# Kernel optimization log

Hardware: AMD Instinct MI355X
Metric: run time of the kernel (lower is better)

The kernel has to match this reference:

```python
import jax, jax.numpy as jnp
import numpy as np

VOC, EMB, C, H, W, ANS = 10000, 300, 24, 8, 8, 1000
HID = 500          # lstm_hidden_size
GH = 100           # g_mlp hidden
B, L = 64, 32
O = H * W          # obj_num
CONCAT = 2 * C + HID  # 548


def setup_inputs() -> dict:
    key = jax.random.key(0)
    ks = jax.random.split(key, 20)
    inp = {}
    inp["sent_batch"] = jax.random.randint(ks[0], (B, L), 0, VOC)
    inp["conv_map_batch"] = jax.random.normal(ks[1], (B, C, H, W), jnp.float32)
    inp["sents_lengths"] = jax.random.randint(ks[2], (B,), 1, L + 1)
    # embedding table with padding_idx=0 zeroed
    emb = jax.random.normal(ks[3], (VOC, EMB), jnp.float32) * 0.02
    inp["embed_table"] = emb.at[0].set(0.0)
    # forward-direction LSTM params (torch gate order i,f,g,o)
    s_ih = 1.0 / np.sqrt(HID)
    inp["W_ih"] = jax.random.uniform(ks[4], (4 * HID, EMB), jnp.float32, -s_ih, s_ih)
    inp["W_hh"] = jax.random.uniform(ks[5], (4 * HID, HID), jnp.float32, -s_ih, s_ih)
    inp["b_ih"] = jax.random.uniform(ks[6], (4 * HID,), jnp.float32, -s_ih, s_ih)
    inp["b_hh"] = jax.random.uniform(ks[7], (4 * HID,), jnp.float32, -s_ih, s_ih)
    # random (non-learned) LSTM initial state, as torch.rand in init_hidden
    inp["h0"] = jax.random.uniform(ks[8], (B, HID), jnp.float32)
    inp["c0"] = jax.random.uniform(ks[9], (B, HID), jnp.float32)
    def lin(k, o, i):
        s = 1.0 / np.sqrt(i)
        kw, kb = jax.random.split(k)
        return (jax.random.uniform(kw, (o, i), jnp.float32, -s, s),
                jax.random.uniform(kb, (o,), jnp.float32, -s, s))
    inp["g1_w"], inp["g1_b"] = lin(ks[10], GH, CONCAT)
    inp["g2_w"], inp["g2_b"] = lin(ks[11], GH, GH)
    inp["f1_w"], inp["f1_b"] = lin(ks[12], GH, GH)
    inp["f2_w"], inp["f2_b"] = lin(ks[13], ANS, GH)
    return inp


def _lstm_final_h(emb, lengths, W_ih, W_hh, b_ih, b_hh, h0, c0):
    # emb: (B, L, EMB); returns final forward hidden at t = length-1 per example
    xs = jnp.swapaxes(emb, 0, 1)  # (L, B, EMB)
    ts = jnp.arange(emb.shape[1])
    bias = b_ih + b_hh
    def step(carry, inp):
        h, c = carry
        xt, t = inp
        gates = xt @ W_ih.T + h @ W_hh.T + bias
        i, f, g, o = jnp.split(gates, 4, axis=-1)
        i, f, o = jax.nn.sigmoid(i), jax.nn.sigmoid(f), jax.nn.sigmoid(o)
        g = jnp.tanh(g)
        c_new = f * c + i * g
        h_new = o * jnp.tanh(c_new)
        m = (t < lengths)[:, None]
        return (jnp.where(m, h_new, h), jnp.where(m, c_new, c)), None
    (h_T, _), _ = jax.lax.scan(step, (h0, c0), (xs, ts))
    return h_T  # (B, HID)


def reference(sent_batch, conv_map_batch, sents_lengths, embed_table,
              W_ih, W_hh, b_ih, b_hh, h0, c0,
              g1_w, g1_b, g2_w, g2_b, f1_w, f1_b, f2_w, f2_b):
    emb = embed_table[sent_batch]  # (B, L, EMB)
    q = _lstm_final_h(emb, sents_lengths, W_ih, W_hh, b_ih, b_hh, h0, c0)  # (B, HID)
    obj = jnp.transpose(conv_map_batch, (0, 2, 3, 1)).reshape(B, O, C)  # (B, O, C)
    # g_mlp layer 1, split to avoid materializing (B, O^2, 548):
    # pair (i,j): cat(q, obj_j, obj_i) -> partial sums broadcast-added
    q_part = q @ g1_w[:, :HID].T                    # (B, GH)
    j_part = obj @ g1_w[:, HID:HID + C].T           # (B, O, GH) -- conv_expand_1 block
    i_part = obj @ g1_w[:, HID + C:].T              # (B, O, GH) -- conv_expand_2 block
    h1 = jax.nn.relu(q_part[:, None, None, :] + i_part[:, :, None, :]
                     + j_part[:, None, :, :] + g1_b)  # (B, O, O, GH)
    h2 = jax.nn.relu(h1 @ g2_w.T + g2_b)              # (B, O, O, GH)
    g_sum = h2.sum(axis=(1, 2))                       # (B, GH)
    f = jax.nn.relu(g_sum @ f1_w.T + f1_b)
    f = jax.nn.relu(f @ f2_w.T + f2_b)                # (B, ANS)
    return jax.nn.log_softmax(f, axis=-1)
```

## Files before the change

### kernel.cpp

```cpp
#include <hip/hip_runtime.h>
#include <cmath>

#define BATCH 64
#define SEQL  32
#define EMBD  300
#define HIDD  500
#define NOBJ  64
#define GHID  100
#define ANSN  1000
#define MCOL  2048

#define GRP    4
#define GBATCH 16
#define BPG    25
#define UPB8   20
#define NBLK   (GRP*BPG)
#define SLOTP  32

#define KPADX  328
#define TCH    4

typedef _Float16 half8 __attribute__((ext_vector_type(8)));
typedef float    f32x4 __attribute__((ext_vector_type(4)));

__device__ __forceinline__ float sigmf(float x){ return 1.f/(1.f+expf(-x)); }

__device__ __forceinline__ unsigned long long ld_cc8(const unsigned long long* p){
    return __hip_atomic_load(p, __ATOMIC_RELAXED, __HIP_MEMORY_SCOPE_AGENT);
}
__device__ __forceinline__ void st_cc8(_Float16* p, unsigned long long v){
    __hip_atomic_store((unsigned long long*)p, v, __ATOMIC_RELAXED, __HIP_MEMORY_SCOPE_AGENT);
}

__global__ __launch_bounds__(256, 1) void k_xg2(
    const int* __restrict__ sent, const float* __restrict__ table,
    const float* __restrict__ Wih, const float* __restrict__ b_ih,
    const float* __restrict__ b_hh, float* __restrict__ xgT, int* __restrict__ slots)
{
    __shared__ _Float16 Sh[64*KPADX];
    __shared__ int sidx[TCH][64];
    int tid = threadIdx.x;
    int tc = blockIdx.x;
    int n0 = blockIdx.y * 64;
    int w = tid >> 6, lane = tid & 63;
    int rA = lane & 15, kb = lane >> 4;

    if (tc == 0 && blockIdx.y == 0 && tid < NBLK)
        __hip_atomic_store(slots + tid*SLOTP, 0, __ATOMIC_RELAXED, __HIP_MEMORY_SCOPE_AGENT);

    for (int i = tid; i < TCH*64; i += 256){
        int tt = i >> 6, b = i & 63;
        sidx[tt][b] = sent[b*SEQL + tc*TCH + tt];
    }
    for (int i = tid; i < 64*75; i += 256){
        int n = i / 75, c4 = i - (i/75)*75;
        float4 v = {0.f,0.f,0.f,0.f};
        if (n0 + n < 2000)
            v = *(const float4*)(Wih + (size_t)(n0+n)*300 + c4*4);
        _Float16* dst = &Sh[n*KPADX + c4*4];
        dst[0]=(_Float16)v.x; dst[1]=(_Float16)v.y; dst[2]=(_Float16)v.z; dst[3]=(_Float16)v.w;
    }
    for (int i = tid; i < 64*20; i += 256){
        int n = i / 20, k = 300 + (i - (i/20)*20);
        Sh[n*KPADX + k] = (_Float16)0.f;
    }
    __syncthreads();
    half8 areg[10];
    #pragma unroll
    for (int ks = 0; ks < 10; ++ks)
        areg[ks] = *(const half8*)&Sh[(w*16 + rA)*KPADX + ks*32 + kb*8];
    float biasr[4];
    #pragma unroll
    for (int r = 0; r < 4; ++r){
        int n = n0 + w*16 + kb*4 + r;
        biasr[r] = (n < 2000) ? b_ih[n] + b_hh[n] : 0.f;
    }
    __syncthreads();

    for (int tt = 0; tt < TCH; ++tt){
        for (int i = tid; i < 64*75; i += 256){
            int m = i / 75, c4 = i - (i/75)*75;
            float4 v = *(const float4*)(table + (size_t)sidx[tt][m]*300 + c4*4);
            _Float16* dst = &Sh[m*KPADX + c4*4];
            dst[0]=(_Float16)v.x; dst[1]=(_Float16)v.y; dst[2]=(_Float16)v.z; dst[3]=(_Float16)v.w;
        }
        for (int i = tid; i < 64*20; i += 256){
            int m = i / 20, k = 300 + (i - (i/20)*20);
            Sh[m*KPADX + k] = (_Float16)0.f;
        }
        __syncthreads();

        f32x4 acc[4] = {};
        #pragma unroll
        for (int ks = 0; ks < 10; ++ks){
            #pragma unroll
            for (int mc = 0; mc < 4; ++mc){
                half8 bf = *(const half8*)&Sh[(mc*16 + rA)*KPADX + ks*32 + kb*8];
                acc[mc] = __builtin_amdgcn_mfma_f32_16x16x32_f16(areg[ks], bf, acc[mc], 0, 0, 0);
            }
        }
        #pragma unroll
        for (int r = 0; r < 4; ++r){
            int n = n0 + w*16 + kb*4 + r;
            if (n < 2000){
                #pragma unroll
                for (int mc = 0; mc < 4; ++mc)
                    xgT[(size_t)n*MCOL + (tc*TCH+tt)*64 + mc*16 + rA] = acc[mc][r] + biasr[r];
            }
        }
        __syncthreads();
    }
}

__device__ __forceinline__ void gbarA(int* slots, int grp, int ub, int seq)
{
    __syncthreads();
    if (threadIdx.x == 0)
        __hip_atomic_store(slots + (grp*BPG + ub)*SLOTP, seq,
                           __ATOMIC_RELAXED, __HIP_MEMORY_SCOPE_AGENT);
    if (threadIdx.x < BPG){
        int* s = slots + (grp*BPG + threadIdx.x)*SLOTP;
        while (__hip_atomic_load(s, __ATOMIC_RELAXED, __HIP_MEMORY_SCOPE_AGENT) < seq)
            __builtin_amdgcn_s_sleep(1);
    }
    asm volatile("" ::: "memory");
    __syncthreads();
}

__global__ __launch_bounds__(320, 1) void k_lstm_v9(
    _Float16* __restrict__ hF, float* __restrict__ hqB,
    const float* __restrict__ xgT, const float* __restrict__ Whh,
    const float* __restrict__ h0, const float* __restrict__ c0,
    const int* __restrict__ lens, int* __restrict__ slots)
{
    __shared__ _Float16 Wl[80*512];
    __shared__ float    gl[4*80*16];
    __shared__ _Float16 hout[16*UPB8];

    int tid = threadIdx.x, bid = blockIdx.x;
    int grp = bid / BPG, ub = bid - grp*BPG;
    int u0  = ub * UPB8;
    int w   = tid >> 6, lane = tid & 63;

    int pb  = tid & 15, puu = tid >> 4;
    int pu  = u0 + puu;
    int gb  = grp*GBATCH + pb;
    float cprev = c0[gb*HIDD + pu];
    float hprev = h0[gb*HIDD + pu];
    int   mylen = lens[gb];
    hout[pb*UPB8 + puu] = (_Float16)hprev;

    for (int i = tid; i < 80*512; i += 320){
        int m = i >> 9, k = i & 511;
        int g = m / UPB8, uu = m - g*UPB8;
        float v = (k < HIDD) ? Whh[(size_t)(g*HIDD + u0 + uu)*HIDD + k] : 0.f;
        int off = (i*2) ^ ((m & 7) << 4);
        *(_Float16*)((char*)Wl + off) = (_Float16)v;
    }
    __syncthreads();
    if (tid < 80){
        int b = tid / 5, q = tid - (tid/5)*5;
        unsigned long long v = *(const unsigned long long*)((const char*)hout + b*40 + q*8);
        st_cc8(hF + ((size_t)(1*GRP + grp)*GBATCH + b)*512 + u0 + q*4, v);
    }
    if (ub == 0 && tid >= 128 && tid < 224){
        int j = tid - 128;
        int buf = j / 48, r = j - buf*48;
        int b = r / 3, q = r - (r/3)*3;
        st_cc8(hF + ((size_t)(buf*GRP + grp)*GBATCH + b)*512 + 500 + q*4, 0ULL);
    }
    gbarA(slots, grp, ub, 1);

    const int mA = lane & 15, kb = lane >> 4;

    for (int t = 0; t < SEQL; ++t){
        const _Float16* hsrc = hF + (size_t)(((t&1)^1)*GRP + grp)*GBATCH*512;

        float xgv[4];
        #pragma unroll
        for (int g = 0; g < 4; ++g)
            xgv[g] = xgT[(size_t)(g*HIDD + pu)*MCOL + t*64 + gb];

        if (w < 4){
            half8 bf[4];
            #pragma unroll
            for (int ks4 = 0; ks4 < 4; ++ks4){
                int ke = (w*4 + ks4)*32 + kb*8;
                const unsigned long long* p =
                    (const unsigned long long*)(hsrc + mA*512 + ke);
                union { unsigned long long q[2]; half8 h; } u;
                u.q[0] = ld_cc8(p);
                u.q[1] = ld_cc8(p + 1);
                bf[ks4] = u.h;
            }
            f32x4 acc[5] = {};
            #pragma unroll
            for (int rt = 0; rt < 5; ++rt){
                #pragma unroll
                for (int ks4 = 0; ks4 < 4; ++ks4){
                    int kByte = (w*4 + ks4)*64 + kb*16;
                    int m = rt*16 + mA;
                    int aOff = (m*1024 + kByte) ^ ((m & 7) << 4);
                    half8 af = *(const half8*)((const char*)Wl + aOff);
                    acc[rt] = __builtin_amdgcn_mfma_f32_16x16x32_f16(af, bf[ks4], acc[rt], 0, 0, 0);
                }
            }
            #pragma unroll
            for (int rt = 0; rt < 5; ++rt)
                #pragma unroll
                for (int r = 0; r < 4; ++r)
                    gl[(w*80 + rt*16 + kb*4 + r)*16 + mA] = acc[rt][r];
        }
        __syncthreads();

        {
            float g4[4];
            #pragma unroll
            for (int g = 0; g < 4; ++g){
                int row = g*UPB8 + puu;
                float s = gl[(0*80 + row)*16 + pb] + gl[(1*80 + row)*16 + pb]
                        + gl[(2*80 + row)*16 + pb] + gl[(3*80 + row)*16 + pb];
                s += xgv[g];
                g4[g] = s;
            }
            float si = sigmf(g4[0]), sf = sigmf(g4[1]);
            float tg = tanhf(g4[2]), so = sigmf(g4[3]);
            float cn = sf*cprev + si*tg;
            float hn = so*tanhf(cn);
            if (t < mylen){ cprev = cn; hprev = hn; }
            hout[pb*UPB8 + puu] = (_Float16)hprev;
            if (t == SEQL-1) hqB[(size_t)gb*512 + pu] = hprev;
        }
        if (t < SEQL-1){
            __syncthreads();
            if (tid < 80){
                int b = tid / 5, q = tid - (tid/5)*5;
                unsigned long long v = *(const unsigned long long*)((const char*)hout + b*40 + q*8);
                st_cc8(hF + ((size_t)((t&1)*GRP + grp)*GBATCH + b)*512 + u0 + q*4, v);
            }
            gbarA(slots, grp, ub, t + 2);
        }
    }
}

__global__ __launch_bounds__(256, 1) void k_pair2(
    const float* __restrict__ hqB, const float* __restrict__ conv,
    const float* __restrict__ g1w, const float* __restrict__ g1b,
    const float* __restrict__ g2w, const float* __restrict__ g2b,
    float* __restrict__ part)
{
    __shared__ float    convl[24][64];
    __shared__ float    g1ij[100][48];
    __shared__ float    hb[512];
    __shared__ float    qpl[112];
    __shared__ float    jpl[NOBJ][132];
    __shared__ float    basel[16][132];
    __shared__ _Float16 g2h[112][136];
    __shared__ float    redx[4][112];

    int b  = blockIdx.x >> 2;
    int ic = blockIdx.x & 3;
    int tid = threadIdx.x;
    int w = tid >> 6, lane = tid & 63;
    int ncol = lane & 15, kb = lane >> 4;

    for (int i = tid; i < 24*64; i += 256)
        convl[i>>6][i&63] = conv[((size_t)b*24 + (i>>6))*64 + (i&63)];
    for (int i = tid; i < 100*48; i += 256){
        int n = i/48, c = i - (i/48)*48;
        g1ij[n][c] = g1w[(size_t)n*548 + 500 + c];
    }
    for (int i = tid; i < 512; i += 256) hb[i] = hqB[(size_t)b*512 + i];
    for (int i = tid; i < 112*136; i += 256){
        int n = i/136, k = i - (i/136)*136;
        g2h[n][k] = (n < 100 && k < 100) ? (_Float16)g2w[n*GHID + k] : (_Float16)0.f;
    }
    __syncthreads();

    if (tid < 100){
        const float4* wr = (const float4*)(g1w + (size_t)tid*548);
        float s = g1b[tid];
        #pragma unroll 5
        for (int k4 = 0; k4 < 125; ++k4){
            float4 v = wr[k4];
            s += v.x*hb[k4*4] + v.y*hb[k4*4+1] + v.z*hb[k4*4+2] + v.w*hb[k4*4+3];
        }
        qpl[tid] = s;
    }
    for (int i = tid; i < NOBJ*100; i += 256){
        int o = i / 100, n = i - (i/100)*100;
        float sj = 0.f;
        #pragma unroll
        for (int c = 0; c < 24; ++c) sj += convl[c][o] * g1ij[n][c];
        jpl[o][n] = sj;
    }
    for (int i = tid; i < NOBJ*32; i += 256) jpl[i>>5][100 + (i&31)] = 0.f;
    __syncthreads();

    for (int i = tid; i < 16*132; i += 256){
        int il = i / 132, k = i - (i/132)*132;
        float v = 0.f;
        if (k < 100){
            float si = 0.f;
            int o = ic*16 + il;
            #pragma unroll
            for (int c = 0; c < 24; ++c) si += convl[c][o] * g1ij[k][24+c];
            v = qpl[k] + si;
        }
        basel[il][k] = v;
    }
    float gb7[7];
    #pragma unroll
    for (int nt = 0; nt < 7; ++nt){
        int n = nt*16 + ncol;
        gb7[nt] = (n < 100) ? g2b[n] : 0.f;
    }
    __syncthreads();

    f32x4 sacc[7] = {};
    #pragma unroll
    for (int it = 0; it < 4; ++it){
        int il = w*4 + it;
        #pragma unroll
        for (int jc = 0; jc < 4; ++jc){
            f32x4 acc[7] = {};
            int jrow = jc*16 + ncol;
            #pragma unroll
            for (int ks = 0; ks < 4; ++ks){
                int k0 = ks*32 + kb*8;
                const float* jpp = &jpl[jrow][k0];
                const float* bpp = &basel[il][k0];
                half8 af;
                #pragma unroll
                for (int e = 0; e < 8; ++e)
                    af[e] = (_Float16)fmaxf(jpp[e] + bpp[e], 0.f);
                #pragma unroll
                for (int nt = 0; nt < 7; ++nt){
                    half8 bf = *(const half8*)&g2h[nt*16 + ncol][k0];
                    acc[nt] = __builtin_amdgcn_mfma_f32_16x16x32_f16(af, bf, acc[nt], 0, 0, 0);
                }
            }
            #pragma unroll
            for (int nt = 0; nt < 7; ++nt)
                #pragma unroll
                for (int r = 0; r < 4; ++r)
                    sacc[nt][r] += fmaxf(acc[nt][r] + gb7[nt], 0.f);
        }
    }
    #pragma unroll
    for (int nt = 0; nt < 7; ++nt){
        float s = sacc[nt][0] + sacc[nt][1] + sacc[nt][2] + sacc[nt][3];
        s += __shfl_xor(s, 16);
        s += __shfl_xor(s, 32);
        if (lane < 16) redx[w][nt*16 + lane] = s;
    }
    __syncthreads();
    if (tid < 100){
        float p = redx[0][tid] + redx[1][tid] + redx[2][tid] + redx[3][tid];
        part[(size_t)(b*4 + ic)*GHID + tid] = p;
    }
}

__global__ __launch_bounds__(256) void k_final(const float* __restrict__ part, const float* __restrict__ f1w,
               const float* __restrict__ f1b, const float* __restrict__ f2w,
               const float* __restrict__ f2b, float* __restrict__ out)
{
    int b = blockIdx.x;
    int tid = threadIdx.x;
    __shared__ float gs[GHID];
    __shared__ float fh[GHID];
    __shared__ float lg[ANSN];
    __shared__ float red[4], red2[4];
    if (tid < GHID){
        float s = 0.f;
        for (int ic = 0; ic < 4; ++ic) s += part[((size_t)b*4 + ic)*GHID + tid];
        gs[tid] = s;
    }
    __syncthreads();
    if (tid < GHID){
        float s = f1b[tid];
        const float* w = f1w + tid*GHID;
        for (int k = 0; k < GHID; ++k) s += gs[k]*w[k];
        fh[tid] = fmaxf(s, 0.f);
    }
    __syncthreads();
    for (int n = tid; n < ANSN; n += 256){
        float s = f2b[n];
        const float* w = f2w + (size_t)n*GHID;
        for (int k = 0; k < GHID; ++k) s += fh[k]*w[k];
        lg[n] = fmaxf(s, 0.f);
    }
    __syncthreads();
    float mx = -1e30f;
    for (int n = tid; n < ANSN; n += 256) mx = fmaxf(mx, lg[n]);
    #pragma unroll
    for (int off = 32; off > 0; off >>= 1) mx = fmaxf(mx, __shfl_xor(mx, off));
    if ((tid & 63) == 0) red[tid >> 6] = mx;
    __syncthreads();
    mx = fmaxf(fmaxf(red[0], red[1]), fmaxf(red[2], red[3]));
    float se = 0.f;
    for (int n = tid; n < ANSN; n += 256) se += expf(lg[n]-mx);
    #pragma unroll
    for (int off = 32; off > 0; off >>= 1) se += __shfl_xor(se, off);
    if ((tid & 63) == 0) red2[tid >> 6] = se;
    __syncthreads();
    se = red2[0]+red2[1]+red2[2]+red2[3];
    float lse = logf(se);
    for (int n = tid; n < ANSN; n += 256) out[(size_t)b*ANSN + n] = lg[n] - mx - lse;
}

extern "C" void kernel_launch(void* const* d_in, const int* in_sizes, int n_in,
                              void* d_out, int out_size, void* d_ws, size_t ws_size,
                              hipStream_t stream)
{
    const int*   sent  = (const int*)  d_in[0];
    const float* conv  = (const float*)d_in[1];
    const int*   lens  = (const int*)  d_in[2];
    const float* table = (const float*)d_in[3];
    const float* W_ih  = (const float*)d_in[4];
    const float* W_hh  = (const float*)d_in[5];
    const float* b_ih  = (const float*)d_in[6];
    const float* b_hh  = (const float*)d_in[7];
    const float* h0    = (const float*)d_in[8];
    const float* c0    = (const float*)d_in[9];
    const float* g1_w  = (const float*)d_in[10];
    const float* g1_b  = (const float*)d_in[11];
    const float* g2_w  = (const float*)d_in[12];
    const float* g2_b  = (const float*)d_in[13];
    const float* f1_w  = (const float*)d_in[14];
    const float* f1_b  = (const float*)d_in[15];
    const float* f2_w  = (const float*)d_in[16];
    const float* f2_b  = (const float*)d_in[17];
    float* out = (float*)d_out;

    float* ws   = (float*)d_ws;
    int*   slots= (int*)d_ws;
    _Float16* hF = (_Float16*)(ws + 16384);
    float* hqB  = ws + 16384 + 32768;
    float* xgT  = hqB + 64*512;
    float* part = xgT + (size_t)4*HIDD*MCOL;

    {
        dim3 g(SEQL/TCH, 32);
        k_xg2<<<g, 256, 0, stream>>>(sent, table, W_ih, b_ih, b_hh, xgT, slots);
    }

    k_lstm_v9<<<NBLK, 320, 0, stream>>>(hF, hqB, xgT, W_hh, h0, c0, lens, slots);

    k_pair2<<<BATCH*4, 256, 0, stream>>>(hqB, conv, g1_w, g1_b, g2_w, g2_b, part);

    k_final<<<BATCH, 256, 0, stream>>>(part, f1_w, f1_b, f2_w, f2_b, out);
}
```

Before: 258.3 us.

## Fuse input-gate GEMM into LSTM kernel with per-chunk readiness flags

Merges the x·W_ih precompute kernel into the persistent LSTM kernel. Extra blocks beyond the 100 recurrence blocks compute the input gates for 4-timestep chunks and bump a per-chunk counter. Recurrence blocks wait on that counter before each chunk, so the input projection overlaps the serial recurrence instead of running before it. The risk is deadlock if the recurrence blocks are not co-resident or are scheduled ahead of the producer blocks. It also adds a memset launch plus atomic loads and stores on xgT.

```diff
diff --git a/kernel.cpp b/kernel.cpp
--- a/kernel.cpp
+++ b/kernel.cpp
@@ -15,6 +15,7 @@
 #define BPG    25
 #define UPB8   20
 #define NBLK   (GRP*BPG)
+#define NXG    256
 #define SLOTP  32
 
 #define KPADX  328
@@ -31,85 +32,11 @@
 __device__ __forceinline__ void st_cc8(_Float16* p, unsigned long long v){
     __hip_atomic_store((unsigned long long*)p, v, __ATOMIC_RELAXED, __HIP_MEMORY_SCOPE_AGENT);
 }
-
-__global__ __launch_bounds__(256, 1) void k_xg2(
-    const int* __restrict__ sent, const float* __restrict__ table,
-    const float* __restrict__ Wih, const float* __restrict__ b_ih,
-    const float* __restrict__ b_hh, float* __restrict__ xgT, int* __restrict__ slots)
-{
-    __shared__ _Float16 Sh[64*KPADX];
-    __shared__ int sidx[TCH][64];
-    int tid = threadIdx.x;
-    int tc = blockIdx.x;
-    int n0 = blockIdx.y * 64;
-    int w = tid >> 6, lane = tid & 63;
-    int rA = lane & 15, kb = lane >> 4;
-
-    if (tc == 0 && blockIdx.y == 0 && tid < NBLK)
-        __hip_atomic_store(slots + tid*SLOTP, 0, __ATOMIC_RELAXED, __HIP_MEMORY_SCOPE_AGENT);
-
-    for (int i = tid; i < TCH*64; i += 256){
-        int tt = i >> 6, b = i & 63;
-        sidx[tt][b] = sent[b*SEQL + tc*TCH + tt];
-    }
-    for (int i = tid; i < 64*75; i += 256){
-        int n = i / 75, c4 = i - (i/75)*75;
-        float4 v = {0.f,0.f,0.f,0.f};
-        if (n0 + n < 2000)
-            v = *(const float4*)(Wih + (size_t)(n0+n)*300 + c4*4);
-        _Float16* dst = &Sh[n*KPADX + c4*4];
-        dst[0]=(_Float16)v.x; dst[1]=(_Float16)v.y; dst[2]=(_Float16)v.z; dst[3]=(_Float16)v.w;
-    }
-    for (int i = tid; i < 64*20; i += 256){
-        int n = i / 20, k = 300 + (i - (i/20)*20);
-        Sh[n*KPADX + k] = (_Float16)0.f;
-    }
-    __syncthreads();
-    half8 areg[10];
-    #pragma unroll
-    for (int ks = 0; ks < 10; ++ks)
-        areg[ks] = *(const half8*)&Sh[(w*16 + rA)*KPADX + ks*32 + kb*8];
-    float biasr[4];
-    #pragma unroll
-    for (int r = 0; r < 4; ++r){
-        int n = n0 + w*16 + kb*4 + r;
-        biasr[r] = (n < 2000) ? b_ih[n] + b_hh[n] : 0.f;
-    }
-    __syncthreads();
-
-    for (int tt = 0; tt < TCH; ++tt){
-        for (int i = tid; i < 64*75; i += 256){
-            int m = i / 75, c4 = i - (i/75)*75;
-            float4 v = *(const float4*)(table + (size_t)sidx[tt][m]*300 + c4*4);
-            _Float16* dst = &Sh[m*KPADX + c4*4];
-            dst[0]=(_Float16)v.x; dst[1]=(_Float16)v.y; dst[2]=(_Float16)v.z; dst[3]=(_Float16)v.w;
-        }
-        for (int i = tid; i < 64*20; i += 256){
-            int m = i / 20, k = 300 + (i - (i/20)*20);
-            Sh[m*KPADX + k] = (_Float16)0.f;
-        }
-        __syncthreads();
-
-        f32x4 acc[4] = {};
-        #pragma unroll
-        for (int ks = 0; ks < 10; ++ks){
-            #pragma unroll
-            for (int mc = 0; mc < 4; ++mc){
-                half8 bf = *(const half8*)&Sh[(mc*16 + rA)*KPADX + ks*32 + kb*8];
-                acc[mc] = __builtin_amdgcn_mfma_f32_16x16x32_f16(areg[ks], bf, acc[mc], 0, 0, 0);
-            }
-        }
-        #pragma unroll
-        for (int r = 0; r < 4; ++r){
-            int n = n0 + w*16 + kb*4 + r;
-            if (n < 2000){
-                #pragma unroll
-                for (int mc = 0; mc < 4; ++mc)
-                    xgT[(size_t)n*MCOL + (tc*TCH+tt)*64 + mc*16 + rA] = acc[mc][r] + biasr[r];
-            }
-        }
-        __syncthreads();
-    }
+__device__ __forceinline__ float ld_cc4(const float* p){
+    return __hip_atomic_load(p, __ATOMIC_RELAXED, __HIP_MEMORY_SCOPE_AGENT);
+}
+__device__ __forceinline__ void st_cc4(float* p, float v){
+    __hip_atomic_store(p, v, __ATOMIC_RELAXED, __HIP_MEMORY_SCOPE_AGENT);
 }
 
 __device__ __forceinline__ void gbarA(int* slots, int grp, int ub, int seq)
@@ -127,20 +54,105 @@
     __syncthreads();
 }
 
-__global__ __launch_bounds__(320, 1) void k_lstm_v9(
-    _Float16* __restrict__ hF, float* __restrict__ hqB,
-    const float* __restrict__ xgT, const float* __restrict__ Whh,
-    const float* __restrict__ h0, const float* __restrict__ c0,
-    const int* __restrict__ lens, int* __restrict__ slots)
+__global__ __launch_bounds__(320, 1) void k_mega(
+    const int* __restrict__ sent, const float* __restrict__ table,
+    const float* __restrict__ Wih, const float* __restrict__ b_ih, const float* __restrict__ b_hh,
+    _Float16* __restrict__ hF, float* __restrict__ hqB, float* __restrict__ xgT,
+    const float* __restrict__ Whh, const float* __restrict__ h0, const float* __restrict__ c0,
+    const int* __restrict__ lens, int* __restrict__ slots, int* __restrict__ xgdone)
 {
-    __shared__ _Float16 Wl[80*512];
-    __shared__ float    gl[4*80*16];
-    __shared__ _Float16 hout[16*UPB8];
+    __shared__ __align__(16) char smem[103040];
 
     int tid = threadIdx.x, bid = blockIdx.x;
+    int w = tid >> 6, lane = tid & 63;
+
+    if (bid >= NBLK){
+        _Float16* Sh  = (_Float16*)smem;
+        int*      sidx= (int*)(smem + 41984);
+        int xb = bid - NBLK;
+        int tc = xb >> 5;
+        int n0 = (xb & 31) * 64;
+        int rA = lane & 15, kb = lane >> 4;
+
+        for (int i = tid; i < TCH*64; i += 320){
+            int tt = i >> 6, b = i & 63;
+            sidx[tt*64 + b] = sent[b*SEQL + tc*TCH + tt];
+        }
+        for (int i = tid; i < 64*75; i += 320){
+            int n = i / 75, c4 = i - (i/75)*75;
+            float4 v = {0.f,0.f,0.f,0.f};
+            if (n0 + n < 2000)
+                v = *(const float4*)(Wih + (size_t)(n0+n)*300 + c4*4);
+            _Float16* dst = &Sh[n*KPADX + c4*4];
+            dst[0]=(_Float16)v.x; dst[1]=(_Float16)v.y; dst[2]=(_Float16)v.z; dst[3]=(_Float16)v.w;
+        }
+        for (int i = tid; i < 64*20; i += 320){
+            int n = i / 20, k = 300 + (i - (i/20)*20);
+            Sh[n*KPADX + k] = (_Float16)0.f;
+        }
+        __syncthreads();
+        half8 areg[10];
+        float biasr[4];
+        if (w < 4){
+            #pragma unroll
+            for (int ks = 0; ks < 10; ++ks)
+                areg[ks] = *(const half8*)&Sh[(w*16 + rA)*KPADX + ks*32 + kb*8];
+            #pragma unroll
+            for (int r = 0; r < 4; ++r){
+                int n = n0 + w*16 + kb*4 + r;
+                biasr[r] = (n < 2000) ? b_ih[n] + b_hh[n] : 0.f;
+            }
+        }
+        __syncthreads();
+
+        for (int tt = 0; tt < TCH; ++tt){
+            for (int i = tid; i < 64*75; i += 320){
+                int m = i / 75, c4 = i - (i/75)*75;
+                float4 v = *(const float4*)(table + (size_t)sidx[tt*64 + m]*300 + c4*4);
+                _Float16* dst = &Sh[m*KPADX + c4*4];
+                dst[0]=(_Float16)v.x; dst[1]=(_Float16)v.y; dst[2]=(_Float16)v.z; dst[3]=(_Float16)v.w;
+            }
+            for (int i = tid; i < 64*20; i += 320){
+                int m = i / 20, k = 300 + (i - (i/20)*20);
+                Sh[m*KPADX + k] = (_Float16)0.f;
+            }
+            __syncthreads();
+
+            if (w < 4){
+                f32x4 acc[4] = {};
+                #pragma unroll
+                for (int ks = 0; ks < 10; ++ks){
+                    #pragma unroll
+                    for (int mc = 0; mc < 4; ++mc){
+                        half8 bf = *(const half8*)&Sh[(mc*16 + rA)*KPADX + ks*32 + kb*8];
+                        acc[mc] = __builtin_amdgcn_mfma_f32_16x16x32_f16(areg[ks], bf, acc[mc], 0, 0, 0);
+                    }
+                }
+                #pragma unroll
+                for (int r = 0; r < 4; ++r){
+                    int n = n0 + w*16 + kb*4 + r;
+                    if (n < 2000){
+                        #pragma unroll
+                        for (int mc = 0; mc < 4; ++mc)
+                            st_cc4(xgT + (size_t)n*MCOL + (tc*TCH+tt)*64 + mc*16 + rA,
+                                   acc[mc][r] + biasr[r]);
+                    }
+                }
+            }
+            __syncthreads();
+        }
+        if (tid == 0)
+            __hip_atomic_fetch_add(xgdone + tc*SLOTP, 1,
+                                   __ATOMIC_RELAXED, __HIP_MEMORY_SCOPE_AGENT);
+        return;
+    }
+
+    _Float16* Wl  = (_Float16*)smem;
+    float*    gl  = (float*)(smem + 81920);
+    _Float16* hout= (_Float16*)(smem + 102400);
+
     int grp = bid / BPG, ub = bid - grp*BPG;
     int u0  = ub * UPB8;
-    int w   = tid >> 6, lane = tid & 63;
 
     int pb  = tid & 15, puu = tid >> 4;
     int pu  = u0 + puu;
@@ -174,12 +186,22 @@
     const int mA = lane & 15, kb = lane >> 4;
 
     for (int t = 0; t < SEQL; ++t){
+        if ((t & 3) == 0){
+            if (tid == 0){
+                const int* f = xgdone + (t >> 2)*SLOTP;
+                while (__hip_atomic_load(f, __ATOMIC_RELAXED, __HIP_MEMORY_SCOPE_AGENT) < 32)
+                    __builtin_amdgcn_s_sleep(1);
+            }
+            asm volatile("" ::: "memory");
+            __syncthreads();
+        }
+
         const _Float16* hsrc = hF + (size_t)(((t&1)^1)*GRP + grp)*GBATCH*512;
 
         float xgv[4];
         #pragma unroll
         for (int g = 0; g < 4; ++g)
-            xgv[g] = xgT[(size_t)(g*HIDD + pu)*MCOL + t*64 + gb];
+            xgv[g] = ld_cc4(xgT + (size_t)(g*HIDD + pu)*MCOL + t*64 + gb);
 
         if (w < 4){
             half8 bf[4];
@@ -433,19 +455,19 @@
     const float* f2_b  = (const float*)d_in[17];
     float* out = (float*)d_out;
 
-    float* ws   = (float*)d_ws;
-    int*   slots= (int*)d_ws;
+    float* ws    = (float*)d_ws;
+    int*   slots = (int*)d_ws;
+    int*   xgdone= (int*)d_ws + NBLK*SLOTP;
     _Float16* hF = (_Float16*)(ws + 16384);
     float* hqB  = ws + 16384 + 32768;
     float* xgT  = hqB + 64*512;
     float* part = xgT + (size_t)4*HIDD*MCOL;
 
-    {
-        dim3 g(SEQL/TCH, 32);
-        k_xg2<<<g, 256, 0, stream>>>(sent, table, W_ih, b_ih, b_hh, xgT, slots);
-    }
-
-    k_lstm_v9<<<NBLK, 320, 0, stream>>>(hF, hqB, xgT, W_hh, h0, c0, lens, slots);
+    hipMemsetAsync(slots, 0, 16384, stream);
+
+    k_mega<<<NBLK + NXG, 320, 0, stream>>>(sent, table, W_ih, b_ih, b_hh,
+                                           hF, hqB, xgT, W_hh, h0, c0, lens,
+                                           slots, xgdone);
 
     k_pair2<<<BATCH*4, 256, 0, stream>>>(hqB, conv, g1_w, g1_b, g2_w, g2_b, part);
 
```

Measured after the change: 226.6 us. -12.3%, faster.
